# Optimization experiments

Hardware: AMD Instinct MI355X
Metric: run time of the kernel (lower is better)

Reference implementation:

```python
import jax, jax.numpy as jnp
import numpy as np

B, NW = 1024, 300
N = NW // 3          # 100 tokens (keypoints)
E = 5                # token dim after cat of PE(2): 3 + 2
H, D, L = 4, 64, 3   # heads, d_attention, layers


def setup_inputs() -> dict:
    key = jax.random.key(0)
    ks = jax.random.split(key, 8)
    s = jnp.float32(0.1)
    x = jax.random.normal(ks[0], (B, NW), dtype=jnp.float32)
    Wq = jax.random.normal(ks[1], (L, H, D, E), dtype=jnp.float32) * s  # per-head W_Q (no bias)
    Wk = jax.random.normal(ks[2], (L, H, D, E), dtype=jnp.float32) * s
    Wv = jax.random.normal(ks[3], (L, H, D, E), dtype=jnp.float32) * s
    Wo = jax.random.normal(ks[4], (L, E, H * D), dtype=jnp.float32) * s  # MHA output proj (no bias)
    Wf = jax.random.normal(ks[5], (L, E, E), dtype=jnp.float32) * s      # FFN linear
    bf = jax.random.normal(ks[6], (L, E), dtype=jnp.float32) * s
    g1 = jnp.ones((L, E), dtype=jnp.float32)
    b1 = jnp.zeros((L, E), dtype=jnp.float32)
    g2 = jnp.ones((L, E), dtype=jnp.float32)
    b2 = jnp.zeros((L, E), dtype=jnp.float32)
    return dict(x=x, Wq=Wq, Wk=Wk, Wv=Wv, Wo=Wo, Wf=Wf, bf=bf,
                g1=g1, b1=b1, g2=g2, b2=b2)


def _layer_norm(x, g, b, eps=1e-5):
    mu = jnp.mean(x, axis=-1, keepdims=True)
    var = jnp.mean((x - mu) ** 2, axis=-1, keepdims=True)  # biased, like torch LN
    return (x - mu) / jnp.sqrt(var + eps) * g + b


def reference(x, Wq, Wk, Wv, Wo, Wf, bf, g1, b1, g2, b2):
    kp = x.reshape(B, N, 3)                      # 'b (n d) -> b n d', d=3
    mask = kp[:, :, -1] > 0                      # [B,N] keypoint confidence mask
    # PositionalEncoding(d_model=2, kind='cat'): div_term=[1] -> pe=[sin(pos),cos(pos)]
    pos = jnp.arange(N, dtype=jnp.float32)
    pe = jnp.stack([jnp.sin(pos), jnp.cos(pos)], axis=-1)         # [N,2]
    out = jnp.concatenate([kp, jnp.broadcast_to(pe, (B, N, 2))], axis=-1)  # [B,N,5]
    out = jnp.where(mask[:, :, None], out, jnp.float32(0.0))      # out[~mask]=0

    pair = mask[:, None, None, :] & mask[:, None, :, None]        # [B,1,N,N]
    neg = -jnp.finfo(jnp.float32).max
    scale = jnp.float32(1.0 / np.sqrt(D))
    for l in range(L):
        # per-head projections (heads vectorized over h)
        q = jnp.einsum('bne,hde->bhnd', out, Wq[l])
        k = jnp.einsum('bne,hde->bhnd', out, Wk[l])
        v = jnp.einsum('bne,hde->bhnd', out, Wv[l])
        dots = jnp.einsum('bhid,bhjd->bhij', q, k) * scale        # [B,H,N,N]
        dots = jnp.where(pair, dots, neg)
        attn = jax.nn.softmax(dots, axis=-1)
        o = jnp.einsum('bhij,bhjd->bhid', attn, v)                # [B,H,N,D]
        o = o.transpose(0, 2, 1, 3).reshape(B, N, H * D)          # concat heads
        attn_out = o @ Wo[l].T                                    # [B,N,E]
        ln1 = _layer_norm(attn_out + out, g1[l], b1[l])
        ffn = jax.nn.relu(ln1 @ Wf[l].T + bf[l])
        out = _layer_norm(ffn + ln1, g2[l], b2[l])
    return out
```

## Files before the change

### kernel.cpp

```cpp
#include <hip/hip_runtime.h>
#include <math.h>

#define NTOK 100
#define EDIM 5
#define NH   4
#define NL   3
#define DD   64
#define BLK  256
#define LOG2E 1.4426950408889634f

__global__ void precompute_mp(const float* __restrict__ Wq,
                              const float* __restrict__ Wk,
                              const float* __restrict__ Wv,
                              const float* __restrict__ Wo,
                              float* __restrict__ mp) {
  const int blk = blockIdx.x;
  const int which = blk / 12;
  const int rem = blk % 12;
  const int l = rem / 4, h = rem % 4;
  const int t = threadIdx.x;

  __shared__ float A[320];
  __shared__ float Bsh[320];

  const float* wa = (which ? Wv : Wq) + (l*NH + h)*DD*EDIM;
  for (int r = t; r < 320; r += 64) A[r] = wa[r];
  if (which == 0) {
    const float* wk = Wk + (l*NH + h)*DD*EDIM;
    for (int r = t; r < 320; r += 64) Bsh[r] = wk[r];
  } else {
    for (int r = t; r < 320; r += 64) {
      int f = r >> 6, d = r & 63;
      Bsh[r] = Wo[(l*EDIM + f)*(NH*DD) + h*DD + d];
    }
  }
  __syncthreads();
  if (t < 25) {
    int e = t / 5, f = t % 5;
    float acc = 0.f;
    if (which == 0) {
      #pragma unroll 8
      for (int d = 0; d < DD; ++d) acc += A[d*5+e] * Bsh[d*5+f];
      acc *= 0.125f;
    } else {
      #pragma unroll 8
      for (int d = 0; d < DD; ++d) acc += A[d*5+e] * Bsh[f*64+d];
    }
    mp[which*960 + ((l*NH + h)*EDIM + e)*8 + f] = acc;
  }
}

__global__ __launch_bounds__(BLK) void encoder_kernel(
    const float* __restrict__ x,
    const float* __restrict__ mp,
    const float* __restrict__ Wf,
    const float* __restrict__ bfv,
    const float* __restrict__ g1,
    const float* __restrict__ b1,
    const float* __restrict__ g2,
    const float* __restrict__ b2,
    float* __restrict__ out)
{
  const int wv   = threadIdx.x >> 6;
  const int lane = threadIdx.x & 63;
  const int b    = blockIdx.x;

  __shared__ float s_mp[1920];
  __shared__ float s_st[104][8];
  __shared__ float s_w[NH][104][8];
  __shared__ int   s_cidx[NTOK];

  for (int r = threadIdx.x; r < 480; r += BLK)
    ((float4*)s_mp)[r] = ((const float4*)mp)[r];

  const float* xb = x + b*300;
  const int t1 = lane, t2 = lane + 64;
  float k0a = xb[3*t1], k1a = xb[3*t1+1], k2a = xb[3*t1+2];
  bool m1 = (k2a > 0.f);
  float k0b = 0.f, k1b = 0.f, k2b = 0.f; bool m2 = false;
  if (t2 < NTOK) {
    k0b = xb[3*t2]; k1b = xb[3*t2+1]; k2b = xb[3*t2+2];
    m2 = (k2b > 0.f);
  }
  unsigned long long bm1 = __ballot(m1);
  unsigned long long bm2 = __ballot(m2);
  const int pc1 = __popcll(bm1);
  const int nm  = pc1 + __popcll(bm2);
  const int ns  = nm + 1;
  if (wv == 0) {
    unsigned long long below = (lane == 0) ? 0ull : ((1ull << lane) - 1ull);
    int p1 = __popcll(bm1 & below);
    int p2 = pc1 + __popcll(bm2 & below);
    if (m1) {
      *(float4*)(&s_st[p1][0]) = make_float4(k0a, k1a, k2a, sinf((float)t1));
      s_st[p1][4] = cosf((float)t1);
    }
    s_cidx[t1] = m1 ? p1 : nm;
    if (t2 < NTOK) {
      if (m2) {
        *(float4*)(&s_st[p2][0]) = make_float4(k0b, k1b, k2b, sinf((float)t2));
        s_st[p2][4] = cosf((float)t2);
      }
      s_cidx[t2] = m2 ? p2 : nm;
    }
    if (lane == 0) {
      *(float4*)(&s_st[nm][0]) = make_float4(0.f,0.f,0.f,0.f);
      s_st[nm][4] = 0.f;
    }
  }
  __syncthreads();

  const int nh2 = (ns > 64) ? 2 : 1;

  for (int l = 0; l < NL; ++l) {
    for (int half = 0; half < nh2; ++half) {
      const int row = lane + (half << 6);
      const bool active = (row < ns);
      const bool rep = (row == nm);
      const int rr = active ? row : 0;

      float4 ov = *(const float4*)(&s_st[rr][0]);
      float o[5] = {ov.x, ov.y, ov.z, ov.w, s_st[rr][4]};

      const float* Mh = s_mp + (l*NH + wv)*40;
      float a0=0.f,a1=0.f,a2=0.f,a3=0.f,a4=0.f;
      #pragma unroll
      for (int e = 0; e < 5; ++e) {
        float4 mr = *(const float4*)(Mh + e*8);
        float  m4 = Mh[e*8+4];
        a0 += o[e]*mr.x; a1 += o[e]*mr.y; a2 += o[e]*mr.z; a3 += o[e]*mr.w; a4 += o[e]*m4;
      }
      a0*=LOG2E; a1*=LOG2E; a2*=LOG2E; a3*=LOG2E; a4*=LOG2E;

      float ls=0.f, w0=0.f,w1=0.f,w2=0.f,w3=0.f,w4=0.f;
      #pragma unroll 4
      for (int j = 0; j < nm; ++j) {
        float4 oj = *(const float4*)(&s_st[j][0]);
        float  oe = s_st[j][4];
        float s = a0*oj.x + a1*oj.y + a2*oj.z + a3*oj.w + a4*oe;
        float p = __builtin_amdgcn_exp2f(s);
        p = rep ? 1.f : p;
        ls += p;
        w0 += p*oj.x; w1 += p*oj.y; w2 += p*oj.z; w3 += p*oj.w; w4 += p*oe;
      }
      if (active) {
        *(float4*)(&s_w[wv][row][0]) = make_float4(w0, w1, w2, w3);
        *(float2*)(&s_w[wv][row][4]) = make_float2(w4, ls);
      }
    }
    __syncthreads();

    if (wv == 0) {
      for (int half = 0; half < nh2; ++half) {
        const int row = lane + (half << 6);
        const bool active = (row < ns);
        const bool rep = (row == nm);
        const int rr = active ? row : 0;

        float4 ov = *(const float4*)(&s_st[rr][0]);
        float o[5] = {ov.x, ov.y, ov.z, ov.w, s_st[rr][4]};
        float wext = rep ? (float)(NTOK - nm) : 0.f;

        float c[5] = {0.f,0.f,0.f,0.f,0.f};
        const float* Pl = s_mp + 960 + l*NH*40;
        #pragma unroll
        for (int h = 0; h < NH; ++h) {
          float4 wa = *(const float4*)(&s_w[h][rr][0]);
          float2 wb = *(const float2*)(&s_w[h][rr][4]);
          float w[5] = {wa.x, wa.y, wa.z, wa.w, wb.x};
          float inv = rep ? 0.01f : 1.f/wb.y;
          const float* Ph = Pl + h*40;
          #pragma unroll
          for (int f = 0; f < 5; ++f) {
            float wn = (w[f] + wext*o[f]) * inv;
            float4 pr = *(const float4*)(Ph + f*8);
            float  p4 = Ph[f*8+4];
            c[0]+=wn*pr.x; c[1]+=wn*pr.y; c[2]+=wn*pr.z; c[3]+=wn*pr.w; c[4]+=wn*p4;
          }
        }
        float y[5];
        #pragma unroll
        for (int e = 0; e < 5; ++e) y[e] = o[e] + c[e];
        float mu = 0.2f*(y[0]+y[1]+y[2]+y[3]+y[4]);
        float var = 0.f;
        #pragma unroll
        for (int e = 0; e < 5; ++e) { float d = y[e]-mu; var += d*d; }
        var *= 0.2f;
        float inv1 = 1.f/sqrtf(var + 1e-5f);
        float ln1[5];
        #pragma unroll
        for (int e = 0; e < 5; ++e) ln1[e] = (y[e]-mu)*inv1*g1[l*5+e] + b1[l*5+e];
        float rv[5];
        #pragma unroll
        for (int e = 0; e < 5; ++e) {
          float acc = bfv[l*5+e];
          #pragma unroll
          for (int f = 0; f < 5; ++f) acc += ln1[f]*Wf[(l*5+e)*5+f];
          acc = acc > 0.f ? acc : 0.f;
          rv[e] = acc + ln1[e];
        }
        float mu2 = 0.2f*(rv[0]+rv[1]+rv[2]+rv[3]+rv[4]);
        float var2 = 0.f;
        #pragma unroll
        for (int e = 0; e < 5; ++e) { float d = rv[e]-mu2; var2 += d*d; }
        var2 *= 0.2f;
        float inv2 = 1.f/sqrtf(var2 + 1e-5f);
        float n0 = (rv[0]-mu2)*inv2*g2[l*5+0] + b2[l*5+0];
        float n1 = (rv[1]-mu2)*inv2*g2[l*5+1] + b2[l*5+1];
        float n2 = (rv[2]-mu2)*inv2*g2[l*5+2] + b2[l*5+2];
        float n3 = (rv[3]-mu2)*inv2*g2[l*5+3] + b2[l*5+3];
        float n4 = (rv[4]-mu2)*inv2*g2[l*5+4] + b2[l*5+4];
        if (active) {
          *(float4*)(&s_st[row][0]) = make_float4(n0, n1, n2, n3);
          s_st[row][4] = n4;
        }
      }
    }
    __syncthreads();
  }

  const int obase = b*(NTOK*EDIM);
  for (int idx = threadIdx.x; idx < NTOK*EDIM; idx += BLK) {
    int tok = idx / 5;
    int e = idx - tok*5;
    int c = s_cidx[tok];
    out[obase + idx] = s_st[c][e];
  }
}

extern "C" void kernel_launch(void* const* d_in, const int* in_sizes, int n_in,
                              void* d_out, int out_size, void* d_ws, size_t ws_size,
                              hipStream_t stream) {
  const float* x  = (const float*)d_in[0];
  const float* Wq = (const float*)d_in[1];
  const float* Wk = (const float*)d_in[2];
  const float* Wv = (const float*)d_in[3];
  const float* Wo = (const float*)d_in[4];
  const float* Wf = (const float*)d_in[5];
  const float* bf = (const float*)d_in[6];
  const float* g1 = (const float*)d_in[7];
  const float* b1 = (const float*)d_in[8];
  const float* g2 = (const float*)d_in[9];
  const float* b2 = (const float*)d_in[10];
  float* outp = (float*)d_out;
  float* mp   = (float*)d_ws;

  precompute_mp<<<24, 64, 0, stream>>>(Wq, Wk, Wv, Wo, mp);
  encoder_kernel<<<1024, BLK, 0, stream>>>(x, mp, Wf, bf, g1, b1, g2, b2, outp);
}
```

Measured before the change: 128.2 us.

## Split attention key loop across two wave groups and parallelize epilogue across waves

The block grows from 256 to 512 threads. Each head is now handled by two waves, each covering half of the key range, and their partial softmax sums are combined in the epilogue. The epilogue also moves from one wave looping over both row halves to one wave per half. This shortens the serial key loop per wave and the single-wave epilogue, at the cost of twice the threads per block, a larger s_w shared buffer and possibly lower occupancy.

```diff
diff --git a/kernel.cpp b/kernel.cpp
--- a/kernel.cpp
+++ b/kernel.cpp
@@ -6,7 +6,7 @@
 #define NH   4
 #define NL   3
 #define DD   64
-#define BLK  256
+#define BLK  512
 #define LOG2E 1.4426950408889634f
 
 __global__ void precompute_mp(const float* __restrict__ Wq,
@@ -63,11 +63,13 @@
 {
   const int wv   = threadIdx.x >> 6;
   const int lane = threadIdx.x & 63;
+  const int hd   = wv & 3;
+  const int jg   = wv >> 2;
   const int b    = blockIdx.x;
 
   __shared__ float s_mp[1920];
   __shared__ float s_st[104][8];
-  __shared__ float s_w[NH][104][8];
+  __shared__ float s_w[2][NH][104][8];
   __shared__ int   s_cidx[NTOK];
 
   for (int r = threadIdx.x; r < 480; r += BLK)
@@ -110,7 +112,10 @@
   }
   __syncthreads();
 
-  const int nh2 = (ns > 64) ? 2 : 1;
+  const int nh2  = (ns > 64) ? 2 : 1;
+  const int jmid = nm >> 1;
+  const int jlo  = jg ? jmid : 0;
+  const int jhi  = jg ? nm : jmid;
 
   for (int l = 0; l < NL; ++l) {
     for (int half = 0; half < nh2; ++half) {
@@ -122,7 +127,7 @@
       float4 ov = *(const float4*)(&s_st[rr][0]);
       float o[5] = {ov.x, ov.y, ov.z, ov.w, s_st[rr][4]};
 
-      const float* Mh = s_mp + (l*NH + wv)*40;
+      const float* Mh = s_mp + (l*NH + hd)*40;
       float a0=0.f,a1=0.f,a2=0.f,a3=0.f,a4=0.f;
       #pragma unroll
       for (int e = 0; e < 5; ++e) {
@@ -134,7 +139,7 @@
 
       float ls=0.f, w0=0.f,w1=0.f,w2=0.f,w3=0.f,w4=0.f;
       #pragma unroll 4
-      for (int j = 0; j < nm; ++j) {
+      for (int j = jlo; j < jhi; ++j) {
         float4 oj = *(const float4*)(&s_st[j][0]);
         float  oe = s_st[j][4];
         float s = a0*oj.x + a1*oj.y + a2*oj.z + a3*oj.w + a4*oe;
@@ -144,87 +149,90 @@
         w0 += p*oj.x; w1 += p*oj.y; w2 += p*oj.z; w3 += p*oj.w; w4 += p*oe;
       }
       if (active) {
-        *(float4*)(&s_w[wv][row][0]) = make_float4(w0, w1, w2, w3);
-        *(float2*)(&s_w[wv][row][4]) = make_float2(w4, ls);
+        *(float4*)(&s_w[jg][hd][row][0]) = make_float4(w0, w1, w2, w3);
+        *(float2*)(&s_w[jg][hd][row][4]) = make_float2(w4, ls);
       }
     }
     __syncthreads();
 
-    if (wv == 0) {
-      for (int half = 0; half < nh2; ++half) {
-        const int row = lane + (half << 6);
-        const bool active = (row < ns);
-        const bool rep = (row == nm);
-        const int rr = active ? row : 0;
-
-        float4 ov = *(const float4*)(&s_st[rr][0]);
-        float o[5] = {ov.x, ov.y, ov.z, ov.w, s_st[rr][4]};
-        float wext = rep ? (float)(NTOK - nm) : 0.f;
-
-        float c[5] = {0.f,0.f,0.f,0.f,0.f};
-        const float* Pl = s_mp + 960 + l*NH*40;
+    if (wv < nh2) {
+      const int row = lane + (wv << 6);
+      const bool active = (row < ns);
+      const bool rep = (row == nm);
+      const int rr = active ? row : 0;
+
+      float4 ov = *(const float4*)(&s_st[rr][0]);
+      float o[5] = {ov.x, ov.y, ov.z, ov.w, s_st[rr][4]};
+      float wext = rep ? (float)(NTOK - nm) : 0.f;
+
+      float c[5] = {0.f,0.f,0.f,0.f,0.f};
+      const float* Pl = s_mp + 960 + l*NH*40;
+      #pragma unroll
+      for (int h = 0; h < NH; ++h) {
+        float4 wa = *(const float4*)(&s_w[0][h][rr][0]);
+        float2 wb = *(const float2*)(&s_w[0][h][rr][4]);
+        float4 wa2 = *(const float4*)(&s_w[1][h][rr][0]);
+        float2 wb2 = *(const float2*)(&s_w[1][h][rr][4]);
+        float w[5] = {wa.x+wa2.x, wa.y+wa2.y, wa.z+wa2.z, wa.w+wa2.w, wb.x+wb2.x};
+        float inv = rep ? 0.01f : 1.f/(wb.y + wb2.y);
+        const float* Ph = Pl + h*40;
         #pragma unroll
-        for (int h = 0; h < NH; ++h) {
-          float4 wa = *(const float4*)(&s_w[h][rr][0]);
-          float2 wb = *(const float2*)(&s_w[h][rr][4]);
-          float w[5] = {wa.x, wa.y, wa.z, wa.w, wb.x};
-          float inv = rep ? 0.01f : 1.f/wb.y;
-          const float* Ph = Pl + h*40;
-          #pragma unroll
-          for (int f = 0; f < 5; ++f) {
-            float wn = (w[f] + wext*o[f]) * inv;
-            float4 pr = *(const float4*)(Ph + f*8);
-            float  p4 = Ph[f*8+4];
-            c[0]+=wn*pr.x; c[1]+=wn*pr.y; c[2]+=wn*pr.z; c[3]+=wn*pr.w; c[4]+=wn*p4;
-          }
+        for (int f = 0; f < 5; ++f) {
+          float wn = (w[f] + wext*o[f]) * inv;
+          float4 pr = *(const float4*)(Ph + f*8);
+          float  p4 = Ph[f*8+4];
+          c[0]+=wn*pr.x; c[1]+=wn*pr.y; c[2]+=wn*pr.z; c[3]+=wn*pr.w; c[4]+=wn*p4;
         }
-        float y[5];
+      }
+      float y[5];
+      #pragma unroll
+      for (int e = 0; e < 5; ++e) y[e] = o[e] + c[e];
+      float mu = 0.2f*(y[0]+y[1]+y[2]+y[3]+y[4]);
+      float var = 0.f;
+      #pragma unroll
+      for (int e = 0; e < 5; ++e) { float d = y[e]-mu; var += d*d; }
+      var *= 0.2f;
+      float inv1 = 1.f/sqrtf(var + 1e-5f);
+      float ln1[5];
+      #pragma unroll
+      for (int e = 0; e < 5; ++e) ln1[e] = (y[e]-mu)*inv1*g1[l*5+e] + b1[l*5+e];
+      float rv[5];
+      #pragma unroll
+      for (int e = 0; e < 5; ++e) {
+        float acc = bfv[l*5+e];
         #pragma unroll
-        for (int e = 0; e < 5; ++e) y[e] = o[e] + c[e];
-        float mu = 0.2f*(y[0]+y[1]+y[2]+y[3]+y[4]);
-        float var = 0.f;
-        #pragma unroll
-        for (int e = 0; e < 5; ++e) { float d = y[e]-mu; var += d*d; }
-        var *= 0.2f;
-        float inv1 = 1.f/sqrtf(var + 1e-5f);
-        float ln1[5];
-        #pragma unroll
-        for (int e = 0; e < 5; ++e) ln1[e] = (y[e]-mu)*inv1*g1[l*5+e] + b1[l*5+e];
-        float rv[5];
-        #pragma unroll
-        for (int e = 0; e < 5; ++e) {
-          float acc = bfv[l*5+e];
-          #pragma unroll
-          for (int f = 0; f < 5; ++f) acc += ln1[f]*Wf[(l*5+e)*5+f];
-          acc = acc > 0.f ? acc : 0.f;
-          rv[e] = acc + ln1[e];
-        }
-        float mu2 = 0.2f*(rv[0]+rv[1]+rv[2]+rv[3]+rv[4]);
-        float var2 = 0.f;
-        #pragma unroll
-        for (int e = 0; e < 5; ++e) { float d = rv[e]-mu2; var2 += d*d; }
-        var2 *= 0.2f;
-        float inv2 = 1.f/sqrtf(var2 + 1e-5f);
-        float n0 = (rv[0]-mu2)*inv2*g2[l*5+0] + b2[l*5+0];
-        float n1 = (rv[1]-mu2)*inv2*g2[l*5+1] + b2[l*5+1];
-        float n2 = (rv[2]-mu2)*inv2*g2[l*5+2] + b2[l*5+2];
-        float n3 = (rv[3]-mu2)*inv2*g2[l*5+3] + b2[l*5+3];
-        float n4 = (rv[4]-mu2)*inv2*g2[l*5+4] + b2[l*5+4];
-        if (active) {
-          *(float4*)(&s_st[row][0]) = make_float4(n0, n1, n2, n3);
-          s_st[row][4] = n4;
-        }
+        for (int f = 0; f < 5; ++f) acc += ln1[f]*Wf[(l*5+e)*5+f];
+        acc = acc > 0.f ? acc : 0.f;
+        rv[e] = acc + ln1[e];
+      }
+      float mu2 = 0.2f*(rv[0]+rv[1]+rv[2]+rv[3]+rv[4]);
+      float var2 = 0.f;
+      #pragma unroll
+      for (int e = 0; e < 5; ++e) { float d = rv[e]-mu2; var2 += d*d; }
+      var2 *= 0.2f;
+      float inv2 = 1.f/sqrtf(var2 + 1e-5f);
+      float n0 = (rv[0]-mu2)*inv2*g2[l*5+0] + b2[l*5+0];
+      float n1 = (rv[1]-mu2)*inv2*g2[l*5+1] + b2[l*5+1];
+      float n2 = (rv[2]-mu2)*inv2*g2[l*5+2] + b2[l*5+2];
+      float n3 = (rv[3]-mu2)*inv2*g2[l*5+3] + b2[l*5+3];
+      float n4 = (rv[4]-mu2)*inv2*g2[l*5+4] + b2[l*5+4];
+      if (active) {
+        *(float4*)(&s_st[row][0]) = make_float4(n0, n1, n2, n3);
+        s_st[row][4] = n4;
       }
     }
     __syncthreads();
   }
 
   const int obase = b*(NTOK*EDIM);
-  for (int idx = threadIdx.x; idx < NTOK*EDIM; idx += BLK) {
-    int tok = idx / 5;
-    int e = idx - tok*5;
-    int c = s_cidx[tok];
-    out[obase + idx] = s_st[c][e];
+  {
+    int idx = threadIdx.x;
+    if (idx < NTOK*EDIM) {
+      int tok = idx / 5;
+      int e = idx - tok*5;
+      int c = s_cidx[tok];
+      out[obase + idx] = s_st[c][e];
+    }
   }
 }
 
```

New measurement: 139.7 us. 9.0% more time.

## Keep token state in registers and broadcast keys via readlane across waves

Applied to the files above, without the earlier changes.

Each wave now holds the compacted token states in registers and broadcasts the key rows with readlane, where before it reloaded them from shared memory in the inner loop. The two halves of the token range are processed together in a single fused loop for the >64 case. Every wave applies its own head's output projection and writes per-head partials to a double-buffered scratch. All waves then redundantly run the layer-norm/FFN token pass, which removes the second barrier and the wave-0-only serial section. The cost is redundant per-token work in every wave and more register pressure.

```diff
diff --git a/kernel.cpp b/kernel.cpp
--- a/kernel.cpp
+++ b/kernel.cpp
@@ -8,6 +8,11 @@
 #define DD   64
 #define BLK  256
 #define LOG2E 1.4426950408889634f
+#define SCR  104
+
+__device__ __forceinline__ float rdlane(float v, int l) {
+  return __int_as_float(__builtin_amdgcn_readlane(__float_as_int(v), l));
+}
 
 __global__ void precompute_mp(const float* __restrict__ Wq,
                               const float* __restrict__ Wk,
@@ -66,9 +71,9 @@
   const int b    = blockIdx.x;
 
   __shared__ float s_mp[1920];
-  __shared__ float s_st[104][8];
-  __shared__ float s_w[NH][104][8];
+  __shared__ float s_st[SCR][8];
   __shared__ int   s_cidx[NTOK];
+  __shared__ float s_c[2*NH*SCR*7];
 
   for (int r = threadIdx.x; r < 480; r += BLK)
     ((float4*)s_mp)[r] = ((const float4*)mp)[r];
@@ -77,28 +82,25 @@
   const int t1 = lane, t2 = lane + 64;
   float k0a = xb[3*t1], k1a = xb[3*t1+1], k2a = xb[3*t1+2];
   bool m1 = (k2a > 0.f);
-  float k0b = 0.f, k1b = 0.f, k2b = 0.f; bool m2 = false;
-  if (t2 < NTOK) {
-    k0b = xb[3*t2]; k1b = xb[3*t2+1]; k2b = xb[3*t2+2];
-    m2 = (k2b > 0.f);
-  }
+  float k0b=0.f, k1b=0.f, k2b=0.f; bool m2=false;
+  if (t2 < NTOK) { k0b=xb[3*t2]; k1b=xb[3*t2+1]; k2b=xb[3*t2+2]; m2=(k2b>0.f); }
   unsigned long long bm1 = __ballot(m1);
   unsigned long long bm2 = __ballot(m2);
   const int pc1 = __popcll(bm1);
   const int nm  = pc1 + __popcll(bm2);
   const int ns  = nm + 1;
   if (wv == 0) {
-    unsigned long long below = (lane == 0) ? 0ull : ((1ull << lane) - 1ull);
+    unsigned long long below = (lane==0) ? 0ull : ((1ull<<lane)-1ull);
     int p1 = __popcll(bm1 & below);
     int p2 = pc1 + __popcll(bm2 & below);
     if (m1) {
-      *(float4*)(&s_st[p1][0]) = make_float4(k0a, k1a, k2a, sinf((float)t1));
+      *(float4*)(&s_st[p1][0]) = make_float4(k0a,k1a,k2a,sinf((float)t1));
       s_st[p1][4] = cosf((float)t1);
     }
     s_cidx[t1] = m1 ? p1 : nm;
     if (t2 < NTOK) {
       if (m2) {
-        *(float4*)(&s_st[p2][0]) = make_float4(k0b, k1b, k2b, sinf((float)t2));
+        *(float4*)(&s_st[p2][0]) = make_float4(k0b,k1b,k2b,sinf((float)t2));
         s_st[p2][4] = cosf((float)t2);
       }
       s_cidx[t2] = m2 ? p2 : nm;
@@ -110,121 +112,180 @@
   }
   __syncthreads();
 
-  const int nh2 = (ns > 64) ? 2 : 1;
+  const bool slow = (ns > 64);
+  const bool act1 = (lane < ns);
+  const bool rep1 = (lane == nm);
+  const int  rA   = act1 ? lane : nm;
+  const int  rBi  = lane + 64;
+  const bool act2 = slow && (rBi < ns);
+  const bool rep2 = (rBi == nm);
+  const int  rB   = act2 ? rBi : nm;
+
+  float o[5], o2[5] = {0.f,0.f,0.f,0.f,0.f};
+  { float4 v = *(const float4*)(&s_st[rA][0]);
+    o[0]=v.x; o[1]=v.y; o[2]=v.z; o[3]=v.w; o[4]=s_st[rA][4]; }
+  if (slow) {
+    float4 v = *(const float4*)(&s_st[rB][0]);
+    o2[0]=v.x; o2[1]=v.y; o2[2]=v.z; o2[3]=v.w; o2[4]=s_st[rB][4];
+  }
 
   for (int l = 0; l < NL; ++l) {
-    for (int half = 0; half < nh2; ++half) {
-      const int row = lane + (half << 6);
-      const bool active = (row < ns);
-      const bool rep = (row == nm);
-      const int rr = active ? row : 0;
-
-      float4 ov = *(const float4*)(&s_st[rr][0]);
-      float o[5] = {ov.x, ov.y, ov.z, ov.w, s_st[rr][4]};
-
-      const float* Mh = s_mp + (l*NH + wv)*40;
-      float a0=0.f,a1=0.f,a2=0.f,a3=0.f,a4=0.f;
+    float* cb = s_c + (l & 1)*(NH*SCR*7);
+    const float* Mh = s_mp + (l*NH + wv)*40;
+    const float* Ph = s_mp + 960 + (l*NH + wv)*40;
+
+    float aA[5] = {0,0,0,0,0}, aB[5] = {0,0,0,0,0};
+    #pragma unroll
+    for (int e = 0; e < 5; ++e) {
+      float4 mr = *(const float4*)(Mh + e*8); float m4 = Mh[e*8+4];
+      aA[0]+=o[e]*mr.x; aA[1]+=o[e]*mr.y; aA[2]+=o[e]*mr.z; aA[3]+=o[e]*mr.w; aA[4]+=o[e]*m4;
+      if (slow) {
+        aB[0]+=o2[e]*mr.x; aB[1]+=o2[e]*mr.y; aB[2]+=o2[e]*mr.z; aB[3]+=o2[e]*mr.w; aB[4]+=o2[e]*m4;
+      }
+    }
+    #pragma unroll
+    for (int e = 0; e < 5; ++e) { aA[e]*=LOG2E; aB[e]*=LOG2E; }
+
+    float wA[5]={0,0,0,0,0}, lsA=0.f;
+    float wB[5]={0,0,0,0,0}, lsB=0.f;
+
+    if (!slow) {
+      #pragma unroll 2
+      for (int j = 0; j < nm; ++j) {
+        float oj[5];
+        #pragma unroll
+        for (int e = 0; e < 5; ++e) oj[e] = rdlane(o[e], j);
+        float s = aA[0]*oj[0]+aA[1]*oj[1]+aA[2]*oj[2]+aA[3]*oj[3]+aA[4]*oj[4];
+        float p = __builtin_amdgcn_exp2f(s);
+        p = rep1 ? 1.f : p;
+        lsA += p;
+        #pragma unroll
+        for (int e = 0; e < 5; ++e) wA[e] += p*oj[e];
+      }
+    } else {
+      #pragma unroll 2
+      for (int j = 0; j < 64; ++j) {
+        float oj[5];
+        #pragma unroll
+        for (int e = 0; e < 5; ++e) oj[e] = rdlane(o[e], j);
+        float sA = aA[0]*oj[0]+aA[1]*oj[1]+aA[2]*oj[2]+aA[3]*oj[3]+aA[4]*oj[4];
+        float sB = aB[0]*oj[0]+aB[1]*oj[1]+aB[2]*oj[2]+aB[3]*oj[3]+aB[4]*oj[4];
+        float pA = __builtin_amdgcn_exp2f(sA);
+        float pB = __builtin_amdgcn_exp2f(sB);
+        pA = rep1 ? 1.f : pA;
+        pB = rep2 ? 1.f : pB;
+        lsA += pA; lsB += pB;
+        #pragma unroll
+        for (int e = 0; e < 5; ++e) { wA[e] += pA*oj[e]; wB[e] += pB*oj[e]; }
+      }
+      for (int j = 64; j < nm; ++j) {
+        float oj[5];
+        #pragma unroll
+        for (int e = 0; e < 5; ++e) oj[e] = rdlane(o2[e], j-64);
+        float sA = aA[0]*oj[0]+aA[1]*oj[1]+aA[2]*oj[2]+aA[3]*oj[3]+aA[4]*oj[4];
+        float sB = aB[0]*oj[0]+aB[1]*oj[1]+aB[2]*oj[2]+aB[3]*oj[3]+aB[4]*oj[4];
+        float pA = __builtin_amdgcn_exp2f(sA);
+        float pB = __builtin_amdgcn_exp2f(sB);
+        pA = rep1 ? 1.f : pA;
+        pB = rep2 ? 1.f : pB;
+        lsA += pA; lsB += pB;
+        #pragma unroll
+        for (int e = 0; e < 5; ++e) { wA[e] += pA*oj[e]; wB[e] += pB*oj[e]; }
+      }
+    }
+
+    {
+      float wext = rep1 ? (float)(NTOK - nm) : 0.f;
+      float inv  = rep1 ? 0.01f : 1.f/lsA;
+      float cc[5] = {0,0,0,0,0};
+      #pragma unroll
+      for (int f = 0; f < 5; ++f) {
+        float wn = (wA[f] + wext*o[f]) * inv;
+        float4 pr = *(const float4*)(Ph + f*8); float p4 = Ph[f*8+4];
+        cc[0]+=wn*pr.x; cc[1]+=wn*pr.y; cc[2]+=wn*pr.z; cc[3]+=wn*pr.w; cc[4]+=wn*p4;
+      }
+      if (act1) {
+        float* dst = cb + (wv*SCR + lane)*7;
+        #pragma unroll
+        for (int e = 0; e < 5; ++e) dst[e] = cc[e];
+      }
+    }
+    if (slow) {
+      float wext = rep2 ? (float)(NTOK - nm) : 0.f;
+      float inv  = rep2 ? 0.01f : 1.f/lsB;
+      float cc[5] = {0,0,0,0,0};
+      #pragma unroll
+      for (int f = 0; f < 5; ++f) {
+        float wn = (wB[f] + wext*o2[f]) * inv;
+        float4 pr = *(const float4*)(Ph + f*8); float p4 = Ph[f*8+4];
+        cc[0]+=wn*pr.x; cc[1]+=wn*pr.y; cc[2]+=wn*pr.z; cc[3]+=wn*pr.w; cc[4]+=wn*p4;
+      }
+      if (act2) {
+        float* dst = cb + (wv*SCR + rBi)*7;
+        #pragma unroll
+        for (int e = 0; e < 5; ++e) dst[e] = cc[e];
+      }
+    }
+    __syncthreads();
+
+    auto tokpass = [&](float* o_, int row) {
+      float sum[5] = {0,0,0,0,0};
+      #pragma unroll
+      for (int h = 0; h < NH; ++h) {
+        const float* src = cb + (h*SCR + row)*7;
+        #pragma unroll
+        for (int e = 0; e < 5; ++e) sum[e] += src[e];
+      }
+      float y[5];
+      #pragma unroll
+      for (int e = 0; e < 5; ++e) y[e] = o_[e] + sum[e];
+      float mu = 0.2f*(y[0]+y[1]+y[2]+y[3]+y[4]);
+      float var = 0.f;
+      #pragma unroll
+      for (int e = 0; e < 5; ++e) { float d = y[e]-mu; var += d*d; }
+      var *= 0.2f;
+      float inv1 = 1.f/sqrtf(var + 1e-5f);
+      float ln1[5];
+      #pragma unroll
+      for (int e = 0; e < 5; ++e) ln1[e] = (y[e]-mu)*inv1*g1[l*5+e] + b1[l*5+e];
+      float rv[5];
       #pragma unroll
       for (int e = 0; e < 5; ++e) {
-        float4 mr = *(const float4*)(Mh + e*8);
-        float  m4 = Mh[e*8+4];
-        a0 += o[e]*mr.x; a1 += o[e]*mr.y; a2 += o[e]*mr.z; a3 += o[e]*mr.w; a4 += o[e]*m4;
-      }
-      a0*=LOG2E; a1*=LOG2E; a2*=LOG2E; a3*=LOG2E; a4*=LOG2E;
-
-      float ls=0.f, w0=0.f,w1=0.f,w2=0.f,w3=0.f,w4=0.f;
-      #pragma unroll 4
-      for (int j = 0; j < nm; ++j) {
-        float4 oj = *(const float4*)(&s_st[j][0]);
-        float  oe = s_st[j][4];
-        float s = a0*oj.x + a1*oj.y + a2*oj.z + a3*oj.w + a4*oe;
-        float p = __builtin_amdgcn_exp2f(s);
-        p = rep ? 1.f : p;
-        ls += p;
-        w0 += p*oj.x; w1 += p*oj.y; w2 += p*oj.z; w3 += p*oj.w; w4 += p*oe;
-      }
-      if (active) {
-        *(float4*)(&s_w[wv][row][0]) = make_float4(w0, w1, w2, w3);
-        *(float2*)(&s_w[wv][row][4]) = make_float2(w4, ls);
-      }
-    }
-    __syncthreads();
-
-    if (wv == 0) {
-      for (int half = 0; half < nh2; ++half) {
-        const int row = lane + (half << 6);
-        const bool active = (row < ns);
-        const bool rep = (row == nm);
-        const int rr = active ? row : 0;
-
-        float4 ov = *(const float4*)(&s_st[rr][0]);
-        float o[5] = {ov.x, ov.y, ov.z, ov.w, s_st[rr][4]};
-        float wext = rep ? (float)(NTOK - nm) : 0.f;
-
-        float c[5] = {0.f,0.f,0.f,0.f,0.f};
-        const float* Pl = s_mp + 960 + l*NH*40;
-        #pragma unroll
-        for (int h = 0; h < NH; ++h) {
-          float4 wa = *(const float4*)(&s_w[h][rr][0]);
-          float2 wb = *(const float2*)(&s_w[h][rr][4]);
-          float w[5] = {wa.x, wa.y, wa.z, wa.w, wb.x};
-          float inv = rep ? 0.01f : 1.f/wb.y;
-          const float* Ph = Pl + h*40;
-          #pragma unroll
-          for (int f = 0; f < 5; ++f) {
-            float wn = (w[f] + wext*o[f]) * inv;
-            float4 pr = *(const float4*)(Ph + f*8);
-            float  p4 = Ph[f*8+4];
-            c[0]+=wn*pr.x; c[1]+=wn*pr.y; c[2]+=wn*pr.z; c[3]+=wn*pr.w; c[4]+=wn*p4;
-          }
-        }
-        float y[5];
-        #pragma unroll
-        for (int e = 0; e < 5; ++e) y[e] = o[e] + c[e];
-        float mu = 0.2f*(y[0]+y[1]+y[2]+y[3]+y[4]);
-        float var = 0.f;
-        #pragma unroll
-        for (int e = 0; e < 5; ++e) { float d = y[e]-mu; var += d*d; }
-        var *= 0.2f;
-        float inv1 = 1.f/sqrtf(var + 1e-5f);
-        float ln1[5];
-        #pragma unroll
-        for (int e = 0; e < 5; ++e) ln1[e] = (y[e]-mu)*inv1*g1[l*5+e] + b1[l*5+e];
-        float rv[5];
-        #pragma unroll
-        for (int e = 0; e < 5; ++e) {
-          float acc = bfv[l*5+e];
-          #pragma unroll
-          for (int f = 0; f < 5; ++f) acc += ln1[f]*Wf[(l*5+e)*5+f];
-          acc = acc > 0.f ? acc : 0.f;
-          rv[e] = acc + ln1[e];
-        }
-        float mu2 = 0.2f*(rv[0]+rv[1]+rv[2]+rv[3]+rv[4]);
-        float var2 = 0.f;
-        #pragma unroll
-        for (int e = 0; e < 5; ++e) { float d = rv[e]-mu2; var2 += d*d; }
-        var2 *= 0.2f;
-        float inv2 = 1.f/sqrtf(var2 + 1e-5f);
-        float n0 = (rv[0]-mu2)*inv2*g2[l*5+0] + b2[l*5+0];
-        float n1 = (rv[1]-mu2)*inv2*g2[l*5+1] + b2[l*5+1];
-        float n2 = (rv[2]-mu2)*inv2*g2[l*5+2] + b2[l*5+2];
-        float n3 = (rv[3]-mu2)*inv2*g2[l*5+3] + b2[l*5+3];
-        float n4 = (rv[4]-mu2)*inv2*g2[l*5+4] + b2[l*5+4];
-        if (active) {
-          *(float4*)(&s_st[row][0]) = make_float4(n0, n1, n2, n3);
-          s_st[row][4] = n4;
-        }
-      }
-    }
-    __syncthreads();
-  }
-
+        float acc = bfv[l*5+e];
+        #pragma unroll
+        for (int f = 0; f < 5; ++f) acc += ln1[f]*Wf[(l*5+e)*5+f];
+        acc = acc > 0.f ? acc : 0.f;
+        rv[e] = acc + ln1[e];
+      }
+      float mu2 = 0.2f*(rv[0]+rv[1]+rv[2]+rv[3]+rv[4]);
+      float var2 = 0.f;
+      #pragma unroll
+      for (int e = 0; e < 5; ++e) { float d = rv[e]-mu2; var2 += d*d; }
+      var2 *= 0.2f;
+      float inv2 = 1.f/sqrtf(var2 + 1e-5f);
+      #pragma unroll
+      for (int e = 0; e < 5; ++e) o_[e] = (rv[e]-mu2)*inv2*g2[l*5+e] + b2[l*5+e];
+    };
+    tokpass(o, rA);
+    if (slow) tokpass(o2, rB);
+  }
+
+  if (wv == 0) {
+    if (act1) {
+      *(float4*)(&s_st[lane][0]) = make_float4(o[0],o[1],o[2],o[3]);
+      s_st[lane][4] = o[4];
+    }
+    if (act2) {
+      *(float4*)(&s_st[rBi][0]) = make_float4(o2[0],o2[1],o2[2],o2[3]);
+      s_st[rBi][4] = o2[4];
+    }
+  }
+  __syncthreads();
   const int obase = b*(NTOK*EDIM);
   for (int idx = threadIdx.x; idx < NTOK*EDIM; idx += BLK) {
     int tok = idx / 5;
     int e = idx - tok*5;
-    int c = s_cidx[tok];
-    out[obase + idx] = s_st[c][e];
+    out[obase + idx] = s_st[s_cidx[tok]][e];
   }
 }
 
```

Result: faster. 123.3 us (-3.8%).
